# Kernel tuning notes

Measured on AMD Instinct MI355X. Metric: run time of the kernel, lower is better.

Reference implementation:

```python
import jax, jax.numpy as jnp
import numpy as np

KH = KW = 3
STRIDE = 1
PAD = 1
DIL = 1


def _bilinear_sample(x, py, px):
    """Zero-padded bilinear sampling.
    x: [B, C, H, W]; py, px: [B, K2, Ho, Wo] float sample coords.
    returns [B, C, K2, Ho, Wo].
    """
    B, C, H, W = x.shape
    y0 = jnp.floor(py)
    x0 = jnp.floor(px)
    wy1 = py - y0
    wx1 = px - x0
    wy0 = 1.0 - wy1
    wx0 = 1.0 - wx1
    xf = x.reshape(B, C, H * W)

    def gather(iy, ix):
        valid = (iy >= 0) & (iy <= H - 1) & (ix >= 0) & (ix <= W - 1)
        iyc = jnp.clip(iy, 0, H - 1).astype(jnp.int32)
        ixc = jnp.clip(ix, 0, W - 1).astype(jnp.int32)
        idx = (iyc * W + ixc).reshape(B, 1, -1)  # [B,1,K2*Ho*Wo]
        v = jnp.take_along_axis(xf, idx, axis=2)
        v = v.reshape(B, C, *iy.shape[1:])
        return v * valid[:, None].astype(x.dtype)

    return (gather(y0, x0) * (wy0 * wx0)[:, None]
            + gather(y0, x0 + 1) * (wy0 * wx1)[:, None]
            + gather(y0 + 1, x0) * (wy1 * wx0)[:, None]
            + gather(y0 + 1, x0 + 1) * (wy1 * wx1)[:, None])


def setup_inputs() -> dict:
    key = jax.random.key(0)
    k1, k2, k3, k4 = jax.random.split(key, 4)
    B, C, H, W = 8, 64, 128, 128
    Cout = 64
    K2 = KH * KW
    x = jax.random.normal(k1, (B, C, H, W), dtype=jnp.float32)
    offset = jax.random.normal(k2, (B, 2 * K2, H, W), dtype=jnp.float32)
    mask = jax.random.uniform(k3, (B, K2, H, W), dtype=jnp.float32)
    n = C * KH * KW
    stdv = 1.0 / np.sqrt(n)
    weight = jax.random.uniform(k4, (Cout, C, KH, KW), dtype=jnp.float32,
                                minval=-stdv, maxval=stdv)
    bias = jnp.zeros((Cout,), dtype=jnp.float32)
    return {"x": x, "offset": offset, "mask": mask, "weight": weight, "bias": bias}


def reference(x, offset, mask, weight, bias):
    B, C, H, W = x.shape
    Cout, Cin, kh, kw = weight.shape
    K2 = kh * kw
    Ho = (H + 2 * PAD - (DIL * (kh - 1) + 1)) // STRIDE + 1
    Wo = (W + 2 * PAD - (DIL * (kw - 1) + 1)) // STRIDE + 1
    # offset channels come interleaved per kernel location: ::2 -> x, 1::2 -> y
    off = offset.reshape(B, K2, 2, Ho, Wo)
    dx = off[:, :, 0]  # [B,K2,Ho,Wo]
    dy = off[:, :, 1]
    base_y = (STRIDE * jnp.arange(Ho) - PAD).astype(x.dtype)  # [Ho]
    base_x = (STRIDE * jnp.arange(Wo) - PAD).astype(x.dtype)  # [Wo]
    ky = (DIL * jnp.arange(kh)).astype(x.dtype)
    kx = (DIL * jnp.arange(kw)).astype(x.dtype)
    koff_y = jnp.repeat(ky, kw)  # [K2]
    koff_x = jnp.tile(kx, kh)    # [K2]
    py = base_y[None, None, :, None] + koff_y[None, :, None, None] + dy
    px = base_x[None, None, None, :] + koff_x[None, :, None, None] + dx
    sampled = _bilinear_sample(x, py, px)          # [B,C,K2,Ho,Wo]
    sampled = sampled * mask[:, None]              # modulation
    w = weight.reshape(Cout, Cin * K2)
    cols = sampled.reshape(B, Cin * K2, Ho, Wo)
    out = jnp.einsum('bqhw,oq->bohw', cols, w) + bias[None, :, None, None]
    return out
```

## Files before the change

### kernel.cpp

```cpp
#include <hip/hip_runtime.h>
#include <hip/hip_bf16.h>
#include <hip/hip_fp16.h>


constexpr int B    = 8;
constexpr int C    = 64;
constexpr int H    = 128;
constexpr int W    = 128;
constexpr int COUT = 64;
constexpr int K2   = 9;
constexpr int HW   = H * W;
constexpr int TPX  = 64;

typedef __attribute__((ext_vector_type(8))) short    short8;
typedef __attribute__((ext_vector_type(8))) _Float16 f16x8;
typedef __attribute__((ext_vector_type(4))) float    f32x4;

constexpr int LDSS = 72;

#define LDS_BARRIER() asm volatile("s_waitcnt lgkmcnt(0)\n\ts_barrier" ::: "memory")

__global__ __launch_bounds__(256) void transpose_x_kernel(
    const float* __restrict__ x, short* __restrict__ xt) {
    __shared__ float tbuf[64][65];
    const int blk  = blockIdx.x;
    const int b    = blk >> 8;
    const int hwb  = (blk & 255) * 64;
    const int lane = threadIdx.x & 63;
    const int grp  = threadIdx.x >> 6;
    const float* xb = x + (size_t)b * C * HW;
#pragma unroll
    for (int r = 0; r < 16; ++r) {
        const int c = grp * 16 + r;
        tbuf[c][lane] = xb[c * HW + hwb + lane];
    }
    __syncthreads();
    short* xo = xt + (size_t)b * HW * C;
#pragma unroll
    for (int r = 0; r < 16; ++r) {
        const int hw_l = grp * 16 + r;
        union { __half h; short s; } u;
        u.h = __float2half(tbuf[lane][hw_l]);
        xo[(size_t)(hwb + hw_l) * C + lane] = u.s;
    }
}

__global__ __launch_bounds__(256) void pack_w_kernel(
    const float* __restrict__ w, short* __restrict__ wfrag) {
    int id = blockIdx.x * blockDim.x + threadIdx.x;
    if (id >= COUT * C * K2) return;
    const int j    = id & 7;
    const int lane = (id >> 3) & 63;
    const int mt   = (id >> 9) & 3;
    const int kk   = (id >> 11) & 1;
    const int k    = id >> 12;
    const int m    = mt * 16 + (lane & 15);
    const int q    = lane >> 4;
    const int c    = kk * 32 + q * 8 + j;
    union { __half h; short s; } u;
    u.h = __float2half(w[(m * C + c) * K2 + k]);
    wfrag[id] = u.s;
}

__global__ __launch_bounds__(512, 4) void mdcn_pc_kernel(
    const short* __restrict__ xt,
    const float* __restrict__ offset,
    const float* __restrict__ mask,
    const short* __restrict__ wfrag,
    const float* __restrict__ bias,
    float* __restrict__ out) {

    __shared__ short   smem[2][TPX * LDSS];
    __shared__ ushort4 pidx[K2 * TPX];
    __shared__ uint2   pwts[K2 * TPX];

    const int wg   = blockIdx.x;
    const int b    = wg & 7;
    const int t    = wg >> 3;
    const int ho   = t >> 1;
    const int px0  = (t & 1) * TPX;

    const int tid  = threadIdx.x;
    const int wave = tid >> 6;

    for (int f = tid; f < K2 * TPX; f += 512) {
        const int k = f >> 6;
        const int i = f & 63;
        const int wo = px0 + i;
        const int ky = k / 3, kx = k % 3;
        const float dx = offset[(((size_t)b * 2 * K2 + 2 * k    ) * H + ho) * W + wo];
        const float dy = offset[(((size_t)b * 2 * K2 + 2 * k + 1) * H + ho) * W + wo];
        const float mm = mask  [(((size_t)b * K2     + k        ) * H + ho) * W + wo];
        const float py = (float)(ho - 1 + ky) + dy;
        const float px = (float)(wo - 1 + kx) + dx;
        const float y0f = floorf(py), x0f = floorf(px);
        const float wy1 = py - y0f,   wx1 = px - x0f;
        const float wy0 = 1.0f - wy1, wx0 = 1.0f - wx1;
        const int iy0 = (int)y0f, ix0 = (int)x0f;
        const int iy1 = iy0 + 1,  ix1 = ix0 + 1;
        const bool vy0 = (iy0 >= 0) & (iy0 < H);
        const bool vy1 = (iy1 >= 0) & (iy1 < H);
        const bool vx0 = (ix0 >= 0) & (ix0 < W);
        const bool vx1 = (ix1 >= 0) & (ix1 < W);
        const float w00 = (vy0 & vx0) ? wy0 * wx0 * mm : 0.0f;
        const float w01 = (vy0 & vx1) ? wy0 * wx1 * mm : 0.0f;
        const float w10 = (vy1 & vx0) ? wy1 * wx0 * mm : 0.0f;
        const float w11 = (vy1 & vx1) ? wy1 * wx1 * mm : 0.0f;
        union { __half2 h2; unsigned u; } p01, p23;
        p01.h2 = __floats2half2_rn(w00, w01);
        p23.h2 = __floats2half2_rn(w10, w11);
        const int cy0 = min(max(iy0, 0), H - 1);
        const int cy1 = min(max(iy1, 0), H - 1);
        const int cx0 = min(max(ix0, 0), W - 1);
        const int cx1 = min(max(ix1, 0), W - 1);
        ushort4 bv;
        bv.x = (unsigned short)(cy0 * W + cx0);
        bv.y = (unsigned short)(cy0 * W + cx1);
        bv.z = (unsigned short)(cy1 * W + cx0);
        bv.w = (unsigned short)(cy1 * W + cx1);
        pidx[f] = bv;
        pwts[f] = uint2{p01.u, p23.u};
    }
    __syncthreads();

    if (wave < 4) {
        const int spx = tid >> 2;
        const int cq  = (tid & 3) * 16;
        const char* xb =
            (const char*)(xt + (size_t)b * HW * C) + cq * 2;

        for (int k = 0; k < K2; ++k) {
            const ushort4 bi = pidx[k * 64 + spx];
            const uint2   wu = pwts[k * 64 + spx];
            union HU { unsigned u; __half2 h2; };
            HU t01{wu.x}, t23{wu.y};
            const __half2 w0 = __half2half2(__low2half (t01.h2));
            const __half2 w1 = __half2half2(__high2half(t01.h2));
            const __half2 w2 = __half2half2(__low2half (t23.h2));
            const __half2 w3 = __half2half2(__high2half(t23.h2));
            const short* s00 = (const short*)(xb + ((int)bi.x << 7));
            const short* s01 = (const short*)(xb + ((int)bi.y << 7));
            const short* s10 = (const short*)(xb + ((int)bi.z << 7));
            const short* s11 = (const short*)(xb + ((int)bi.w << 7));

            short* dst = &smem[k & 1][spx * LDSS + cq];
#pragma unroll
            for (int h = 0; h < 2; ++h) {
                union U8 { short8 s; __half2 h2[4]; };
                const U8 g00{*(const short8*)(s00 + h * 8)};
                const U8 g01{*(const short8*)(s01 + h * 8)};
                const U8 g10{*(const short8*)(s10 + h * 8)};
                const U8 g11{*(const short8*)(s11 + h * 8)};
                U8 rr;
#pragma unroll
                for (int p = 0; p < 4; ++p) {
                    rr.h2[p] = __hfma2(g11.h2[p], w3,
                               __hfma2(g10.h2[p], w2,
                               __hfma2(g01.h2[p], w1,
                               __hmul2(g00.h2[p], w0))));
                }
                *(short8*)(dst + h * 8) = rr.s;
            }
            LDS_BARRIER();
        }
    } else {
        const int w    = wave - 4;
        const int lane = tid & 63;
        const int col  = lane & 15;
        const int q    = lane >> 4;
        const f16x8* wf = (const f16x8*)wfrag;

        f16x8 af[K2][2];
#pragma unroll
        for (int k = 0; k < K2; ++k)
#pragma unroll
            for (int kk = 0; kk < 2; ++kk)
                af[k][kk] = wf[(k * 8 + kk * 4 + w) * 64 + lane];

        f32x4 acc[4];
#pragma unroll
        for (int nt = 0; nt < 4; ++nt) acc[nt] = (f32x4)0.0f;

#pragma unroll
        for (int k = 0; k < K2; ++k) {
            LDS_BARRIER();
#pragma unroll
            for (int kk = 0; kk < 2; ++kk) {
#pragma unroll
                for (int nt = 0; nt < 4; ++nt) {
                    const f16x8 bfrag = *(const f16x8*)(
                        &smem[k & 1][(nt * 16 + col) * LDSS + kk * 32 + q * 8]);
                    acc[nt] = __builtin_amdgcn_mfma_f32_16x16x32_f16(
                        af[k][kk], bfrag, acc[nt], 0, 0, 0);
                }
            }
        }

#pragma unroll
        for (int nt = 0; nt < 4; ++nt) {
            const int wo = px0 + nt * 16 + col;
#pragma unroll
            for (int r = 0; r < 4; ++r) {
                const int o = w * 16 + q * 4 + r;
                out[(((size_t)b * COUT + o) * H + ho) * W + wo] =
                    acc[nt][r] + bias[o];
            }
        }
    }
}

__global__ __launch_bounds__(256) void mdcn_direct_kernel(
    const float* __restrict__ x, const float* __restrict__ offset,
    const float* __restrict__ mask, const float* __restrict__ wsrc,
    const float* __restrict__ bias, float* __restrict__ out) {
    const int p  = blockIdx.x * blockDim.x + threadIdx.x;
    const int wo = p & (W - 1);
    const int ho = (p >> 7) & (H - 1);
    const int b  = p >> 14;
    float acc[COUT];
#pragma unroll
    for (int o = 0; o < COUT; ++o) acc[o] = bias[o];
    const float* xb = x + b * C * HW;
    for (int k = 0; k < K2; ++k) {
        const int ky = k / 3, kx = k % 3;
        const float dx = offset[((b * 2 * K2 + 2 * k    ) * H + ho) * W + wo];
        const float dy = offset[((b * 2 * K2 + 2 * k + 1) * H + ho) * W + wo];
        const float m  = mask  [((b * K2     + k        ) * H + ho) * W + wo];
        const float py = (float)(ho - 1 + ky) + dy;
        const float px = (float)(wo - 1 + kx) + dx;
        const float y0f = floorf(py), x0f = floorf(px);
        const float wy1 = py - y0f, wx1 = px - x0f;
        const float wy0 = 1.0f - wy1, wx0 = 1.0f - wx1;
        const int iy0 = (int)y0f, ix0 = (int)x0f;
        const int iy1 = iy0 + 1, ix1 = ix0 + 1;
        const bool vy0 = (iy0 >= 0) & (iy0 < H);
        const bool vy1 = (iy1 >= 0) & (iy1 < H);
        const bool vx0 = (ix0 >= 0) & (ix0 < W);
        const bool vx1 = (ix1 >= 0) & (ix1 < W);
        const float w00 = (vy0 & vx0) ? wy0 * wx0 * m : 0.0f;
        const float w01 = (vy0 & vx1) ? wy0 * wx1 * m : 0.0f;
        const float w10 = (vy1 & vx0) ? wy1 * wx0 * m : 0.0f;
        const float w11 = (vy1 & vx1) ? wy1 * wx1 * m : 0.0f;
        const int cy0 = min(max(iy0, 0), H - 1);
        const int cy1 = min(max(iy1, 0), H - 1);
        const int cx0 = min(max(ix0, 0), W - 1);
        const int cx1 = min(max(ix1, 0), W - 1);
        const int o00 = cy0 * W + cx0, o01 = cy0 * W + cx1;
        const int o10 = cy1 * W + cx0, o11 = cy1 * W + cx1;
        for (int c = 0; c < C; ++c) {
            const float* xp = xb + c * HW;
            const float val = w00 * xp[o00] + w01 * xp[o01] +
                              w10 * xp[o10] + w11 * xp[o11];
#pragma unroll
            for (int o = 0; o < COUT; ++o)
                acc[o] += wsrc[(o * C + c) * K2 + k] * val;
        }
    }
    float* op = out + ((size_t)b * COUT) * HW + ho * W + wo;
#pragma unroll
    for (int o = 0; o < COUT; ++o) op[o * HW] = acc[o];
}

extern "C" void kernel_launch(void* const* d_in, const int* in_sizes, int n_in,
                              void* d_out, int out_size, void* d_ws, size_t ws_size,
                              hipStream_t stream) {
    const float* x      = (const float*)d_in[0];
    const float* offset = (const float*)d_in[1];
    const float* mask   = (const float*)d_in[2];
    const float* weight = (const float*)d_in[3];
    const float* bias   = (const float*)d_in[4];
    float* out          = (float*)d_out;

    const size_t xt_bytes = (size_t)B * HW * C * sizeof(short);
    const size_t wf_bytes = (size_t)COUT * C * K2 * sizeof(short);
    if (ws_size >= xt_bytes + wf_bytes) {
        short* xt    = (short*)d_ws;
        short* wfrag = (short*)((char*)d_ws + xt_bytes);
        transpose_x_kernel<<<B * (HW / 64), 256, 0, stream>>>(x, xt);
        pack_w_kernel<<<(COUT * C * K2 + 255) / 256, 256, 0, stream>>>(weight, wfrag);
        mdcn_pc_kernel<<<2 * B * H, 512, 0, stream>>>(xt, offset, mask, wfrag, bias, out);
    } else {
        mdcn_direct_kernel<<<(B * HW) / 256, 256, 0, stream>>>(
            x, offset, mask, weight, bias, out);
    }
}
```

Measured before the change: 133.4 us.

## Halve pixel tile to 32 with 256-thread blocks and stream weight fragments

Shrinks the per-block pixel tile from 64 to 32, uses 256-thread blocks (2 gather waves, 2 MFMA waves) and launches four times as many blocks. Each MFMA wave now covers two output-channel tiles and two pixel tiles. Weight fragments are double-buffered per kernel tap instead of all held in registers up front. The aim is lower register and LDS use per block and higher occupancy to hide gather latency, at the cost of reloading weight fragments per tap and more blocks recomputing per-block setup.

```diff
diff --git a/kernel.cpp b/kernel.cpp
--- a/kernel.cpp
+++ b/kernel.cpp
@@ -10,7 +10,7 @@
 constexpr int COUT = 64;
 constexpr int K2   = 9;
 constexpr int HW   = H * W;
-constexpr int TPX  = 64;
+constexpr int TPX  = 32;
 
 typedef __attribute__((ext_vector_type(8))) short    short8;
 typedef __attribute__((ext_vector_type(8))) _Float16 f16x8;
@@ -62,7 +62,7 @@
     wfrag[id] = u.s;
 }
 
-__global__ __launch_bounds__(512, 4) void mdcn_pc_kernel(
+__global__ __launch_bounds__(256, 8) void mdcn_pc_kernel(
     const short* __restrict__ xt,
     const float* __restrict__ offset,
     const float* __restrict__ mask,
@@ -77,15 +77,15 @@
     const int wg   = blockIdx.x;
     const int b    = wg & 7;
     const int t    = wg >> 3;
-    const int ho   = t >> 1;
-    const int px0  = (t & 1) * TPX;
+    const int ho   = t >> 2;
+    const int px0  = (t & 3) * TPX;
 
     const int tid  = threadIdx.x;
     const int wave = tid >> 6;
 
-    for (int f = tid; f < K2 * TPX; f += 512) {
-        const int k = f >> 6;
-        const int i = f & 63;
+    for (int f = tid; f < K2 * TPX; f += 256) {
+        const int k = f >> 5;
+        const int i = f & 31;
         const int wo = px0 + i;
         const int ky = k / 3, kx = k % 3;
         const float dx = offset[(((size_t)b * 2 * K2 + 2 * k    ) * H + ho) * W + wo];
@@ -123,15 +123,15 @@
     }
     __syncthreads();
 
-    if (wave < 4) {
+    if (wave < 2) {
         const int spx = tid >> 2;
         const int cq  = (tid & 3) * 16;
         const char* xb =
             (const char*)(xt + (size_t)b * HW * C) + cq * 2;
 
         for (int k = 0; k < K2; ++k) {
-            const ushort4 bi = pidx[k * 64 + spx];
-            const uint2   wu = pwts[k * 64 + spx];
+            const ushort4 bi = pidx[k * TPX + spx];
+            const uint2   wu = pwts[k * TPX + spx];
             union HU { unsigned u; __half2 h2; };
             HU t01{wu.x}, t23{wu.y};
             const __half2 w0 = __half2half2(__low2half (t01.h2));
@@ -164,46 +164,63 @@
             LDS_BARRIER();
         }
     } else {
-        const int w    = wave - 4;
+        const int w    = wave - 2;
         const int lane = tid & 63;
         const int col  = lane & 15;
         const int q    = lane >> 4;
         const f16x8* wf = (const f16x8*)wfrag;
 
-        f16x8 af[K2][2];
-#pragma unroll
-        for (int k = 0; k < K2; ++k)
+        f32x4 acc[2][2];
+#pragma unroll
+        for (int m = 0; m < 2; ++m)
+#pragma unroll
+            for (int n = 0; n < 2; ++n) acc[m][n] = (f32x4)0.0f;
+
+        f16x8 afa[4], afb[4];
+#pragma unroll
+        for (int m = 0; m < 2; ++m)
 #pragma unroll
             for (int kk = 0; kk < 2; ++kk)
-                af[k][kk] = wf[(k * 8 + kk * 4 + w) * 64 + lane];
-
-        f32x4 acc[4];
-#pragma unroll
-        for (int nt = 0; nt < 4; ++nt) acc[nt] = (f32x4)0.0f;
+                afa[m * 2 + kk] = wf[(kk * 4 + 2 * w + m) * 64 + lane];
 
 #pragma unroll
         for (int k = 0; k < K2; ++k) {
+            auto& af  = (k & 1) ? afb : afa;
+            auto& afn = (k & 1) ? afa : afb;
             LDS_BARRIER();
+            if (k + 1 < K2) {
+#pragma unroll
+                for (int m = 0; m < 2; ++m)
+#pragma unroll
+                    for (int kk = 0; kk < 2; ++kk)
+                        afn[m * 2 + kk] =
+                            wf[((k + 1) * 8 + kk * 4 + 2 * w + m) * 64 + lane];
+            }
 #pragma unroll
             for (int kk = 0; kk < 2; ++kk) {
 #pragma unroll
-                for (int nt = 0; nt < 4; ++nt) {
+                for (int n = 0; n < 2; ++n) {
                     const f16x8 bfrag = *(const f16x8*)(
-                        &smem[k & 1][(nt * 16 + col) * LDSS + kk * 32 + q * 8]);
-                    acc[nt] = __builtin_amdgcn_mfma_f32_16x16x32_f16(
-                        af[k][kk], bfrag, acc[nt], 0, 0, 0);
+                        &smem[k & 1][(n * 16 + col) * LDSS + kk * 32 + q * 8]);
+#pragma unroll
+                    for (int m = 0; m < 2; ++m)
+                        acc[m][n] = __builtin_amdgcn_mfma_f32_16x16x32_f16(
+                            af[m * 2 + kk], bfrag, acc[m][n], 0, 0, 0);
                 }
             }
         }
 
 #pragma unroll
-        for (int nt = 0; nt < 4; ++nt) {
-            const int wo = px0 + nt * 16 + col;
-#pragma unroll
-            for (int r = 0; r < 4; ++r) {
-                const int o = w * 16 + q * 4 + r;
-                out[(((size_t)b * COUT + o) * H + ho) * W + wo] =
-                    acc[nt][r] + bias[o];
+        for (int m = 0; m < 2; ++m) {
+#pragma unroll
+            for (int n = 0; n < 2; ++n) {
+                const int wo = px0 + n * 16 + col;
+#pragma unroll
+                for (int r = 0; r < 4; ++r) {
+                    const int o = (2 * w + m) * 16 + q * 4 + r;
+                    out[(((size_t)b * COUT + o) * H + ho) * W + wo] =
+                        acc[m][n][r] + bias[o];
+                }
             }
         }
     }
@@ -278,7 +295,7 @@
         short* wfrag = (short*)((char*)d_ws + xt_bytes);
         transpose_x_kernel<<<B * (HW / 64), 256, 0, stream>>>(x, xt);
         pack_w_kernel<<<(COUT * C * K2 + 255) / 256, 256, 0, stream>>>(weight, wfrag);
-        mdcn_pc_kernel<<<2 * B * H, 512, 0, stream>>>(xt, offset, mask, wfrag, bias, out);
+        mdcn_pc_kernel<<<4 * B * H, 256, 0, stream>>>(xt, offset, mask, wfrag, bias, out);
     } else {
         mdcn_direct_kernel<<<(B * HW) / 256, 256, 0, stream>>>(
             x, offset, mask, weight, bias, out);
```

New measurement: 136.8 us. 1.03x slower.
